# Performance work log

Hardware: AMD Instinct MI355X
Metric: run time of the kernel (lower is better)

Reference implementation:

```python
import jax, jax.numpy as jnp
import numpy as np

K = 16      # neighbors per node (hard-coded in ParticleNet)
EPS = 1e-5  # BatchNorm eps


def _forward(x, convs, fcW1, fcb1, fcW2, fcb2):
    # x: [B, N, F0]; convs: list of 3 layer-lists of (W, b, gamma, beta)
    B, N, _ = x.shape
    for c, layers in enumerate(convs):
        feat = x[..., :2] if c == 0 else x            # first kNN uses coords only
        sq = jnp.sum(feat * feat, axis=-1)            # [B, N]
        d2 = sq[:, :, None] + sq[:, None, :] - 2.0 * jnp.einsum('bnf,bmf->bnm', feat, feat)
        d2 = d2 + jnp.eye(N, dtype=d2.dtype) * 1e9    # exclude self-loops (knn_graph loop=False)
        idx = jax.lax.top_k(-d2, K)[1]                # [B, N, K] nearest-neighbor indices
        x_j = jax.vmap(lambda xb, ib: xb[ib])(x, idx) # gather neighbors -> [B, N, K, F]
        x_i = jnp.broadcast_to(x[:, :, None, :], x_j.shape)
        h = jnp.concatenate([x_i, x_j - x_i], axis=-1)  # PyG EdgeConv message input
        for (W, b, g, e) in layers:                   # Linear -> BatchNorm1d(train) -> ReLU
            h = h @ W + b
            m = h.mean(axis=(0, 1, 2))
            v = h.var(axis=(0, 1, 2))
            h = jax.nn.relu(g * (h - m) * jax.lax.rsqrt(v + EPS) + e)
        x = jnp.concatenate([h.mean(axis=2), x], axis=-1)  # aggr='mean', then skip-concat
    pooled = x.mean(axis=1)                           # global_mean_pool -> [B, 451]
    return (pooled @ fcW1 + fcb1) @ fcW2 + fcb2       # fc1 (no act) then fc2


def setup_inputs() -> dict:
    key = jax.random.key(0)
    B, N, F = 128, 128, 3
    ins, outs = [6, 134, 390], [64, 128, 256]
    d = {}
    ki = [0]
    def nk():
        ki[0] += 1
        return jax.random.fold_in(key, ki[0])
    d['x'] = jax.random.normal(nk(), (B, N, F), jnp.float32)
    for c in range(3):
        dims = [(ins[c], outs[c]), (outs[c], outs[c]), (outs[c], outs[c])]
        for l, (fi, fo) in enumerate(dims):
            d[f'W{c}{l}'] = jax.random.normal(nk(), (fi, fo), jnp.float32) / np.sqrt(fi).astype(np.float32)
            d[f'b{c}{l}'] = jnp.zeros((fo,), jnp.float32)
            d[f'g{c}{l}'] = jnp.ones((fo,), jnp.float32)
            d[f'e{c}{l}'] = jnp.zeros((fo,), jnp.float32)
    d['fcW1'] = jax.random.normal(nk(), (451, 256), jnp.float32) / np.float32(np.sqrt(451))
    d['fcb1'] = jnp.zeros((256,), jnp.float32)
    d['fcW2'] = jax.random.normal(nk(), (256, 5), jnp.float32) / np.float32(np.sqrt(256))
    d['fcb2'] = jnp.zeros((5,), jnp.float32)
    return d


def reference(x,
              W00, b00, g00, e00, W01, b01, g01, e01, W02, b02, g02, e02,
              W10, b10, g10, e10, W11, b11, g11, e11, W12, b12, g12, e12,
              W20, b20, g20, e20, W21, b21, g21, e21, W22, b22, g22, e22,
              fcW1, fcb1, fcW2, fcb2):
    convs = [
        [(W00, b00, g00, e00), (W01, b01, g01, e01), (W02, b02, g02, e02)],
        [(W10, b10, g10, e10), (W11, b11, g11, e11), (W12, b12, g12, e12)],
        [(W20, b20, g20, e20), (W21, b21, g21, e21), (W22, b22, g22, e22)],
    ]
    return _forward(x, convs, fcW1, fcb1, fcW2, fcb2)
```

## Files before the change

### kernel.cpp

```cpp
#include <hip/hip_runtime.h>
#include <hip/hip_bf16.h>
#include <type_traits>

typedef __hip_bfloat16 bf16;
typedef short v8s __attribute__((ext_vector_type(8)));
typedef short v2s __attribute__((ext_vector_type(2)));
typedef float v4f __attribute__((ext_vector_type(4)));

__device__ __forceinline__ float b2f(bf16 v) { return __bfloat162float(v); }
__device__ __forceinline__ bf16  f2b(float v) { return __float2bfloat16(v); }
__device__ __forceinline__ short f2bs(float v) {
    bf16 b = f2b(v); short s; __builtin_memcpy(&s, &b, 2); return s;
}
__device__ __forceinline__ float bs2f(short s) {
    bf16 b; __builtin_memcpy(&b, &s, 2); return b2f(b);
}

#define NB 128
#define NN 128
#define KNN 16
#define M_NODES (NB * NN)
#define NPOS ((long)M_NODES * KNN)
#define NREP 16

__device__ __forceinline__ void fold_stats(const float* __restrict__ st, int c,
                                           float& sum, float& sq) {
    sum = 0.f; sq = 0.f;
#pragma unroll
    for (int r = 0; r < NREP; ++r) { sum += st[r * 512 + c]; sq += st[r * 512 + 256 + c]; }
}

template<int TPB>
__device__ __forceinline__ int swz_tile(int bid) {
    int xcd = bid & 7;
    int slot = bid >> 3;
    int batch = xcd * 16 + slot / TPB;
    int tile = slot - (slot / TPB) * TPB;
    return batch * TPB + tile;
}

__global__ __launch_bounds__(256) void prep_kernel(
    const float* __restrict__ W0, const float* __restrict__ W1, const float* __restrict__ W2,
    short* __restrict__ W0d, short* __restrict__ W0b,
    short* __restrict__ W1b, short* __restrict__ W2b,
    float* __restrict__ stats, int F, int Fpad, int O)
{
    int i = blockIdx.x * 256 + threadIdx.x;
    const int nz = 3 * NREP * 512;
    if (i < nz) { stats[i] = 0.f; return; }
    i -= nz;
    const int n0 = O * Fpad;
    if (i < n0) {
        int c = i / Fpad, k = i - c * Fpad;
        if (k < F) {
            float wt = W0[(size_t)k * O + c];
            float wb = W0[(size_t)(F + k) * O + c];
            W0d[i] = f2bs(wt - wb);
            W0b[i] = f2bs(wb);
        } else { W0d[i] = 0; W0b[i] = 0; }
        return;
    }
    i -= n0;
    const int n1 = O * O;
    if (i < n1) {
        int c = i / O, k = i - c * O;
        W1b[i] = f2bs(W1[(size_t)k * O + c]);
        return;
    }
    i -= n1;
    if (i < n1) {
        int c = i / O, k = i - c * O;
        W2b[i] = f2bs(W2[(size_t)k * O + c]);
    }
}

__global__ __launch_bounds__(256) void dist_kernel(const float* __restrict__ x, int C, int D,
                                                   float* __restrict__ d2) {
    __shared__ float As[16][65];
    __shared__ float Bs[16][65];
    const int tid = threadIdx.x;
    const int tx = tid & 15, ty = tid >> 4;
    const int m0 = blockIdx.y * 64;
    const int b  = m0 >> 7;
    const int c0 = blockIdx.x * 64;
    float acc[4][4], rn[4], cn[4];
#pragma unroll
    for (int r = 0; r < 4; ++r) { rn[r] = 0.f; cn[r] = 0.f;
#pragma unroll
        for (int c = 0; c < 4; ++c) acc[r][c] = 0.f; }
    for (int k0 = 0; k0 < D; k0 += 16) {
        for (int l = tid; l < 1024; l += 256) {
            int k = l & 15, m = l >> 4;
            int kk = k0 + k;
            As[k][m] = (kk < D) ? x[(size_t)(m0 + m) * C + kk] : 0.f;
            Bs[k][m] = (kk < D) ? x[(size_t)(b * NN + c0 + m) * C + kk] : 0.f;
        }
        __syncthreads();
        for (int k = 0; k < 16; ++k) {
            float av[4], bv[4];
#pragma unroll
            for (int r = 0; r < 4; ++r) { av[r] = As[k][ty + 16 * r]; rn[r] += av[r] * av[r]; }
#pragma unroll
            for (int c = 0; c < 4; ++c) { bv[c] = Bs[k][tx + 16 * c]; cn[c] += bv[c] * bv[c]; }
#pragma unroll
            for (int r = 0; r < 4; ++r)
#pragma unroll
                for (int c = 0; c < 4; ++c) acc[r][c] += av[r] * bv[c];
        }
        __syncthreads();
    }
#pragma unroll
    for (int r = 0; r < 4; ++r)
#pragma unroll
        for (int c = 0; c < 4; ++c) {
            int m = m0 + ty + 16 * r;
            int jl = c0 + tx + 16 * c;
            int jg = b * NN + jl;
            float v = rn[r] + cn[c] - 2.0f * acc[r][c];
            if (m == jg) v += 1e9f;
            d2[(size_t)m * NN + jl] = v;
        }
}

__global__ __launch_bounds__(256) void knn_select_kernel(const float* __restrict__ d2,
                                                         int* __restrict__ idx) {
    const int node = blockIdx.x * 4 + (threadIdx.x >> 6);
    const int lane = threadIdx.x & 63;
    const float* row = d2 + (size_t)node * NN;
    float v0 = row[lane], v1 = row[lane + 64];
    int j0 = lane, j1 = lane + 64;
    int myIdx = 0;
#pragma unroll
    for (int k = 0; k < KNN; ++k) {
        float bv; int bj;
        if (v1 < v0 || (v1 == v0 && j1 < j0)) { bv = v1; bj = j1; }
        else                                 { bv = v0; bj = j0; }
#pragma unroll
        for (int off = 32; off; off >>= 1) {
            float ov = __shfl_xor(bv, off);
            int oj = __shfl_xor(bj, off);
            if (ov < bv || (ov == bv && oj < bj)) { bv = ov; bj = oj; }
        }
        if (bj == j0) v0 = 3.0e38f;
        if (bj == j1) v1 = 3.0e38f;
        if (lane == k) myIdx = bj;
    }
    if (lane < KNN) idx[(size_t)node * KNN + lane] = myIdx;
}

template<int O>
__global__ __launch_bounds__(256, 2) void node_gemm_mfma(
    const float* __restrict__ x, int F, int Fpad,
    const short* __restrict__ Wd, const short* __restrict__ Wb,
    const float* __restrict__ bias,
    float* __restrict__ T1, float* __restrict__ T2)
{
    constexpr int CPW = O / 64;
    __shared__ __align__(16) short Am[64][232];
    const int tid = threadIdx.x;
    const int lane = tid & 63, wave = tid >> 6;
    const int l15 = lane & 15, quad = lane >> 4;
    const int m0 = blockIdx.x * 64;
    for (int l = tid; l < 64 * Fpad; l += 256) {
        int m = l / Fpad, k = l - m * Fpad;
        Am[m][k] = (k < F) ? f2bs(x[(size_t)(m0 + m) * F + k]) : (short)0;
    }
    __syncthreads();
#pragma unroll
    for (int p = 0; p < 2; ++p) {
        const short* __restrict__ Wg = p ? Wb : Wd;
        float* __restrict__ T = p ? T2 : T1;
        v4f acc[4][CPW];
#pragma unroll
        for (int rt = 0; rt < 4; ++rt)
#pragma unroll
            for (int j = 0; j < CPW; ++j)
#pragma unroll
                for (int r = 0; r < 4; ++r) acc[rt][j][r] = 0.f;
        for (int k0 = 0; k0 < Fpad; k0 += 32) {
#pragma unroll
            for (int rt = 0; rt < 4; ++rt) {
                v8s av = *(const v8s*)&Am[rt * 16 + l15][k0 + quad * 8];
#pragma unroll
                for (int j = 0; j < CPW; ++j) {
                    int c = (wave * CPW + j) * 16 + l15;
                    v8s bv = *(const v8s*)&Wg[(size_t)c * Fpad + k0 + quad * 8];
                    acc[rt][j] = __builtin_amdgcn_mfma_f32_16x16x32_bf16(av, bv, acc[rt][j], 0, 0, 0);
                }
            }
        }
#pragma unroll
        for (int j = 0; j < CPW; ++j) {
            int c = (wave * CPW + j) * 16 + l15;
            float bb = p ? 0.f : bias[c];
#pragma unroll
            for (int rt = 0; rt < 4; ++rt)
#pragma unroll
                for (int r = 0; r < 4; ++r)
                    T[(size_t)(m0 + rt * 16 + quad * 4 + r) * O + c] = acc[rt][j][r] + bb;
        }
    }
}

template<int O>
__global__ __launch_bounds__(256) void stats0_lds_kernel(
    const float* __restrict__ T1, const float* __restrict__ T2,
    const int* __restrict__ idx, float* __restrict__ st0)
{
    constexpr int CH = (O > 128) ? 128 : O;
    constexpr int NG = 256 / CH;
    constexpr int NPG = NN / NG;
    __shared__ float T2s[NN][CH];
    __shared__ int idxs[NN * KNN];
    __shared__ float redS[NG][CH], redQ[NG][CH];
    const int tid = threadIdx.x;
    const int nchunk = O / CH;
    const int b = blockIdx.x / nchunk;
    const int c0 = (blockIdx.x - b * nchunk) * CH;
    const int rep = blockIdx.x & (NREP - 1);

    for (int l = tid; l < NN * CH; l += 256) {
        int n = l / CH, c = l - n * CH;
        T2s[n][c] = T2[(size_t)(b * NN + n) * O + c0 + c];
    }
    for (int l = tid; l < NN * KNN; l += 256) idxs[l] = idx[(size_t)b * NN * KNN + l];
    __syncthreads();

    const int c = tid & (CH - 1);
    const int g = tid / CH;
    float s = 0.f, q = 0.f;
    for (int n = g * NPG; n < (g + 1) * NPG; ++n) {
        float t1 = T1[(size_t)(b * NN + n) * O + c0 + c];
#pragma unroll
        for (int k = 0; k < KNN; ++k) {
            int j = idxs[n * KNN + k];
            float v = t1 + T2s[j][c];
            s += v; q += v * v;
        }
    }
    redS[g][c] = s; redQ[g][c] = q;
    __syncthreads();
    if (g == 0) {
#pragma unroll
        for (int gg = 1; gg < NG; ++gg) { s += redS[gg][c]; q += redQ[gg][c]; }
        atomicAdd(&st0[rep * 512 + c0 + c], s);
        atomicAdd(&st0[rep * 512 + 256 + c0 + c], q);
    }
}


template<int O, int ROWS>
__global__ __launch_bounds__(256, 4) void gemm1_kernel(
    const float* __restrict__ T1, const float* __restrict__ T2, const int* __restrict__ idx,
    const short* __restrict__ W1, const float* __restrict__ bias1,
    const float* __restrict__ gm0, const float* __restrict__ bt0,
    const float* __restrict__ st0, float* __restrict__ st1,
    short* __restrict__ h, float inv_n)
{
    constexpr int CPW = O / 64;
    constexpr int RT = ROWS / 16;
    constexpr int OSH = (O == 64) ? 6 : (O == 128 ? 7 : 8);
    constexpr int AP = O + 8;
    constexpr int TPB = 2048 / ROWS;
    __shared__ __align__(16) short Am[ROWS][AP];
    __shared__ float sc0[O], sh0[O];
    __shared__ int gArr[ROWS];
    const int tid = threadIdx.x;
    const int lane = tid & 63, wave = tid >> 6;
    const int l15 = lane & 15, quad = lane >> 4;
    const int work = swz_tile<TPB>(blockIdx.x);
    const int e0 = work * ROWS;
    const int nb0 = e0 >> 4;
    const int rep = work & (NREP - 1);

    for (int l = tid; l < ROWS; l += 256) {
        int e = e0 + l;
        int nd = e >> 4;
        gArr[l] = ((nd >> 7) << 7) + idx[e];
    }
    if (tid < O) {
        float sum, sq;
        fold_stats(st0, tid, sum, sq);
        float mean = sum * inv_n;
        float var = fmaxf(sq * inv_n - mean * mean, 0.f);
        float s = rsqrtf(var + 1e-5f) * gm0[tid];
        sc0[tid] = s; sh0[tid] = bt0[tid] - mean * s;
    }
    __syncthreads();

    for (int l = tid; l < ROWS * O / 2; l += 256) {
        int m = l >> (OSH - 1);
        int c = (l & (O / 2 - 1)) * 2;
        const float2 t1 = *(const float2*)&T1[(size_t)(nb0 + (m >> 4)) * O + c];
        const float2 t2 = *(const float2*)&T2[(size_t)gArr[m] * O + c];
        float v0 = fmaxf((t1.x + t2.x) * sc0[c] + sh0[c], 0.f);
        float v1 = fmaxf((t1.y + t2.y) * sc0[c + 1] + sh0[c + 1], 0.f);
        v2s pr; pr[0] = f2bs(v0); pr[1] = f2bs(v1);
        *(v2s*)&Am[m][c] = pr;
    }
    __syncthreads();

    v4f acc[RT][CPW];
#pragma unroll
    for (int rt = 0; rt < RT; ++rt)
#pragma unroll
        for (int j = 0; j < CPW; ++j)
#pragma unroll
            for (int r = 0; r < 4; ++r) acc[rt][j][r] = 0.f;

    v8s bvc[CPW];
#pragma unroll
    for (int j = 0; j < CPW; ++j) {
        int c = (wave * CPW + j) * 16 + l15;
        bvc[j] = *(const v8s*)&W1[(size_t)c * O + quad * 8];
    }
#pragma unroll
    for (int k0 = 0; k0 < O; k0 += 32) {
        v8s bvn[CPW];
        if (k0 + 32 < O) {
#pragma unroll
            for (int j = 0; j < CPW; ++j) {
                int c = (wave * CPW + j) * 16 + l15;
                bvn[j] = *(const v8s*)&W1[(size_t)c * O + k0 + 32 + quad * 8];
            }
        }
#pragma unroll
        for (int rt = 0; rt < RT; ++rt) {
            v8s av = *(const v8s*)&Am[rt * 16 + l15][k0 + quad * 8];
#pragma unroll
            for (int j = 0; j < CPW; ++j)
                acc[rt][j] = __builtin_amdgcn_mfma_f32_16x16x32_bf16(av, bvc[j], acc[rt][j], 0, 0, 0);
        }
        if (k0 + 32 < O) {
#pragma unroll
            for (int j = 0; j < CPW; ++j) bvc[j] = bvn[j];
        }
    }
#pragma unroll
    for (int j = 0; j < CPW; ++j) {
        float bb = bias1[(wave * CPW + j) * 16 + l15];
#pragma unroll
        for (int rt = 0; rt < RT; ++rt)
#pragma unroll
            for (int r = 0; r < 4; ++r) acc[rt][j][r] += bb;
    }
#pragma unroll
    for (int j = 0; j < CPW; ++j) {
        int c = (wave * CPW + j) * 16 + l15;
        float s = 0.f, q = 0.f;
#pragma unroll
        for (int rt = 0; rt < RT; ++rt)
#pragma unroll
            for (int r = 0; r < 4; ++r) { float v = acc[rt][j][r]; s += v; q += v * v; }
        s += __shfl_down(s, 32); s += __shfl_down(s, 16);
        q += __shfl_down(q, 32); q += __shfl_down(q, 16);
        if (quad == 0) { atomicAdd(&st1[rep * 512 + c], s); atomicAdd(&st1[rep * 512 + 256 + c], q); }
    }
    __syncthreads();
#pragma unroll
    for (int j = 0; j < CPW; ++j) {
        int c = (wave * CPW + j) * 16 + l15;
#pragma unroll
        for (int rt = 0; rt < RT; ++rt)
#pragma unroll
            for (int r = 0; r < 4; ++r)
                Am[rt * 16 + quad * 4 + r][c] = f2bs(acc[rt][j][r]);
    }
    __syncthreads();
    for (int g = tid; g < ROWS * O / 8; g += 256) {
        int row = g >> (OSH - 3);
        int c8 = (g & (O / 8 - 1)) * 8;
        *(v8s*)&h[(size_t)(e0 + row) * O + c8] = *(const v8s*)&Am[row][c8];
    }
}

template<int O, int ROWS>
__global__ __launch_bounds__(256, 4) void gemm2_kernel(
    short* __restrict__ h,
    const short* __restrict__ W2, const float* __restrict__ bias2,
    const float* __restrict__ gm1, const float* __restrict__ bt1,
    const float* __restrict__ st1, float* __restrict__ st2, float inv_n)
{
    constexpr int CPW = O / 64;
    constexpr int RT = ROWS / 16;
    constexpr int OSH = (O == 64) ? 6 : (O == 128 ? 7 : 8);
    constexpr int AP = O + 8;
    constexpr int TPB = 2048 / ROWS;
    __shared__ __align__(16) short Am[ROWS][AP];
    __shared__ float sc1[O], sh1[O];
    const int tid = threadIdx.x;
    const int lane = tid & 63, wave = tid >> 6;
    const int l15 = lane & 15, quad = lane >> 4;
    const int work = swz_tile<TPB>(blockIdx.x);
    const int e0 = work * ROWS;
    const int rep = work & (NREP - 1);

    if (tid < O) {
        float sum, sq;
        fold_stats(st1, tid, sum, sq);
        float mean = sum * inv_n;
        float var = fmaxf(sq * inv_n - mean * mean, 0.f);
        float s = rsqrtf(var + 1e-5f) * gm1[tid];
        sc1[tid] = s; sh1[tid] = bt1[tid] - mean * s;
    }
    __syncthreads();

    for (int g = tid; g < ROWS * O / 8; g += 256) {
        int row = g >> (OSH - 3);
        int c8 = (g & (O / 8 - 1)) * 8;
        v8s hv = *(const v8s*)&h[(size_t)(e0 + row) * O + c8];
        v8s ov;
#pragma unroll
        for (int j = 0; j < 8; ++j) {
            float v = bs2f(hv[j]) * sc1[c8 + j] + sh1[c8 + j];
            ov[j] = f2bs(fmaxf(v, 0.f));
        }
        *(v8s*)&Am[row][c8] = ov;
    }
    __syncthreads();

    v4f acc[RT][CPW];
#pragma unroll
    for (int rt = 0; rt < RT; ++rt)
#pragma unroll
        for (int j = 0; j < CPW; ++j)
#pragma unroll
            for (int r = 0; r < 4; ++r) acc[rt][j][r] = 0.f;

    v8s bvc[CPW];
#pragma unroll
    for (int j = 0; j < CPW; ++j) {
        int c = (wave * CPW + j) * 16 + l15;
        bvc[j] = *(const v8s*)&W2[(size_t)c * O + quad * 8];
    }
#pragma unroll
    for (int k0 = 0; k0 < O; k0 += 32) {
        v8s bvn[CPW];
        if (k0 + 32 < O) {
#pragma unroll
            for (int j = 0; j < CPW; ++j) {
                int c = (wave * CPW + j) * 16 + l15;
                bvn[j] = *(const v8s*)&W2[(size_t)c * O + k0 + 32 + quad * 8];
            }
        }
#pragma unroll
        for (int rt = 0; rt < RT; ++rt) {
            v8s av = *(const v8s*)&Am[rt * 16 + l15][k0 + quad * 8];
#pragma unroll
            for (int j = 0; j < CPW; ++j)
                acc[rt][j] = __builtin_amdgcn_mfma_f32_16x16x32_bf16(av, bvc[j], acc[rt][j], 0, 0, 0);
        }
        if (k0 + 32 < O) {
#pragma unroll
            for (int j = 0; j < CPW; ++j) bvc[j] = bvn[j];
        }
    }
#pragma unroll
    for (int j = 0; j < CPW; ++j) {
        float bb = bias2[(wave * CPW + j) * 16 + l15];
#pragma unroll
        for (int rt = 0; rt < RT; ++rt)
#pragma unroll
            for (int r = 0; r < 4; ++r) acc[rt][j][r] += bb;
    }
#pragma unroll
    for (int j = 0; j < CPW; ++j) {
        int c = (wave * CPW + j) * 16 + l15;
        float s = 0.f, q = 0.f;
#pragma unroll
        for (int rt = 0; rt < RT; ++rt)
#pragma unroll
            for (int r = 0; r < 4; ++r) { float v = acc[rt][j][r]; s += v; q += v * v; }
        s += __shfl_down(s, 32); s += __shfl_down(s, 16);
        q += __shfl_down(q, 32); q += __shfl_down(q, 16);
        if (quad == 0) { atomicAdd(&st2[rep * 512 + c], s); atomicAdd(&st2[rep * 512 + 256 + c], q); }
    }
    __syncthreads();
#pragma unroll
    for (int j = 0; j < CPW; ++j) {
        int c = (wave * CPW + j) * 16 + l15;
#pragma unroll
        for (int rt = 0; rt < RT; ++rt)
#pragma unroll
            for (int r = 0; r < 4; ++r)
                Am[rt * 16 + quad * 4 + r][c] = f2bs(acc[rt][j][r]);
    }
    __syncthreads();
    for (int g = tid; g < ROWS * O / 8; g += 256) {
        int row = g >> (OSH - 3);
        int c8 = (g & (O / 8 - 1)) * 8;
        *(v8s*)&h[(size_t)(e0 + row) * O + c8] = *(const v8s*)&Am[row][c8];
    }
}

template<int O, int ROWS>
__global__ __launch_bounds__(256) void finish_kernel(
    const short* __restrict__ h,
    const float* __restrict__ st2, const float* __restrict__ gm2, const float* __restrict__ bt2,
    const float* __restrict__ xold, float* __restrict__ xnew, int F, float inv_n)
{
    constexpr int G = 256 / O;
    constexpr int RPG = ROWS / G;
    constexpr int NPG = RPG / 16;
    constexpr int NPB = ROWS / 16;
    constexpr int TPB = 2048 / ROWS;
    const int tid = threadIdx.x;
    const int c = tid & (O - 1);
    const int rg = tid / O;
    const int work = swz_tile<TPB>(blockIdx.x);
    const int e0 = work * ROWS;
    const int nb0 = e0 >> 4;
    float sum, sq;
    fold_stats(st2, c, sum, sq);
    float mean = sum * inv_n;
    float var = fmaxf(sq * inv_n - mean * mean, 0.f);
    float sc = rsqrtf(var + 1e-5f) * gm2[c];
    float sh = bt2[c] - mean * sc;
    float s[NPG];
#pragma unroll
    for (int i = 0; i < NPG; ++i) s[i] = 0.f;
    const int m0 = rg * RPG;
#pragma unroll
    for (int r = 0; r < RPG; ++r) {
        float v = bs2f(h[(size_t)(e0 + m0 + r) * O + c]) * sc + sh;
        s[r >> 4] += fmaxf(v, 0.f);
    }
    const int Cnew = O + F;
#pragma unroll
    for (int i = 0; i < NPG; ++i)
        xnew[(size_t)(nb0 + rg * NPG + i) * Cnew + c] = s[i] * (1.0f / 16.0f);
    for (int l = tid; l < NPB * F; l += 256) {
        int nd = l / F, cc = l - nd * F;
        xnew[(size_t)(nb0 + nd) * Cnew + O + cc] = xold[(size_t)(nb0 + nd) * F + cc];
    }
}

__global__ __launch_bounds__(256) void pool_kernel(const float* __restrict__ x, float* __restrict__ pooled, int C) {
    int b = blockIdx.x, t = threadIdx.x;
    for (int c = t; c < C; c += 256) {
        float s = 0.f;
        for (int n = 0; n < NN; ++n) s += x[(size_t)(b * NN + n) * C + c];
        pooled[b * C + c] = s * (1.0f / NN);
    }
}

__global__ __launch_bounds__(256) void fc_kernel(const float* __restrict__ pooled,
                                                 const float* __restrict__ W1, const float* __restrict__ b1,
                                                 const float* __restrict__ W2, const float* __restrict__ b2,
                                                 float* __restrict__ out, int C) {
    __shared__ float px[451];
    __shared__ float h1[256];
    int b = blockIdx.x, t = threadIdx.x;
    for (int c = t; c < C; c += 256) px[c] = pooled[b * C + c];
    __syncthreads();
    float s = 0.f;
    for (int i = 0; i < C; ++i) s += px[i] * W1[(size_t)i * 256 + t];
    h1[t] = s + b1[t];
    __syncthreads();
    if (t < 5) {
        float s2 = 0.f;
        for (int j = 0; j < 256; ++j) s2 += h1[j] * W2[j * 5 + t];
        out[b * 5 + t] = s2 + b2[t];
    }
}

extern "C" void kernel_launch(void* const* d_in, const int* in_sizes, int n_in,
                              void* d_out, int out_size, void* d_ws, size_t ws_size,
                              hipStream_t stream) {
    const float* xin = (const float*)d_in[0];
    auto Wp = [&](int c, int l) { return (const float*)d_in[1 + c * 12 + l * 4 + 0]; };
    auto Bp = [&](int c, int l) { return (const float*)d_in[1 + c * 12 + l * 4 + 1]; };
    auto Gp = [&](int c, int l) { return (const float*)d_in[1 + c * 12 + l * 4 + 2]; };
    auto Ep = [&](int c, int l) { return (const float*)d_in[1 + c * 12 + l * 4 + 3]; };
    const float* fcW1 = (const float*)d_in[37];
    const float* fcb1 = (const float*)d_in[38];
    const float* fcW2 = (const float*)d_in[39];
    const float* fcb2 = (const float*)d_in[40];

    char* ws = (char*)d_ws;
    size_t off = 0;
    auto alloc = [&](size_t bytes) -> void* {
        void* p = ws + off;
        off += (bytes + 255) & ~(size_t)255;
        return p;
    };
    const int M = M_NODES;
    float* x1     = (float*)alloc((size_t)M * 67 * 4);
    float* x2     = (float*)alloc((size_t)M * 195 * 4);
    float* x3     = (float*)alloc((size_t)M * 451 * 4);
    float* T1     = (float*)alloc((size_t)M * 256 * 4);
    float* T2     = (float*)alloc((size_t)M * 256 * 4);
    int*   idxb   = (int*)alloc((size_t)M * KNN * 4);
    float* stats  = (float*)alloc((size_t)3 * NREP * 512 * 4);
    float* pooled = (float*)alloc((size_t)NB * 451 * 4);
    short* W1b    = (short*)alloc(256 * 256 * 2);
    short* W2b    = (short*)alloc(256 * 256 * 2);
    short* W0d    = (short*)alloc(256 * 224 * 2);
    short* W0b    = (short*)alloc(256 * 224 * 2);
    float* d2buf  = (float*)alloc((size_t)M * NN * 4);
    short* hbuf   = (short*)alloc((size_t)NPOS * 256 * 2);
    (void)in_sizes; (void)n_in; (void)out_size; (void)ws_size;

    float* st0 = stats;
    float* st1 = stats + NREP * 512;
    float* st2 = stats + 2 * NREP * 512;
    const float inv_n = 1.0f / (float)NPOS;

    auto run_conv = [&](const float* xc, float* xn, int F, int D, int O, int c) {
        const int Fpad = (F + 31) & ~31;
        dist_kernel<<<dim3(2, M / 64), 256, 0, stream>>>(xc, F, D, d2buf);
        knn_select_kernel<<<M / 4, 256, 0, stream>>>(d2buf, idxb);
        const int prepN = 3 * NREP * 512 + O * Fpad + 2 * O * O;
        prep_kernel<<<(prepN + 255) / 256, 256, 0, stream>>>(Wp(c, 0), Wp(c, 1), Wp(c, 2),
            W0d, W0b, W1b, W2b, stats, F, Fpad, O);
        auto launch = [&](auto tag) {
            constexpr int OO = decltype(tag)::value;
            constexpr int RR = 16384 / OO;
            const int grid = (int)(NPOS / RR);
            node_gemm_mfma<OO><<<M / 64, 256, 0, stream>>>(xc, F, Fpad, W0d, W0b, Bp(c, 0), T1, T2);
            stats0_lds_kernel<OO><<<NB * (OO > 128 ? 2 : 1), 256, 0, stream>>>(T1, T2, idxb, st0);
            gemm1_kernel<OO, RR><<<grid, 256, 0, stream>>>(T1, T2, idxb, W1b, Bp(c, 1),
                Gp(c, 0), Ep(c, 0), st0, st1, hbuf, inv_n);
            gemm2_kernel<OO, RR><<<grid, 256, 0, stream>>>(hbuf, W2b, Bp(c, 2),
                Gp(c, 1), Ep(c, 1), st1, st2, inv_n);
            finish_kernel<OO, RR><<<grid, 256, 0, stream>>>(hbuf, st2, Gp(c, 2), Ep(c, 2),
                xc, xn, F, inv_n);
        };
        if (O == 64)       launch(std::integral_constant<int, 64>{});
        else if (O == 128) launch(std::integral_constant<int, 128>{});
        else               launch(std::integral_constant<int, 256>{});
    };

    run_conv(xin, x1, 3, 2, 64, 0);
    run_conv(x1, x2, 67, 67, 128, 1);
    run_conv(x2, x3, 195, 195, 256, 2);
    pool_kernel<<<NB, 256, 0, stream>>>(x3, pooled, 451);
    fc_kernel<<<NB, 256, 0, stream>>>(pooled, fcW1, fcb1, fcW2, fcb2, (float*)d_out, 451);
}
```

Baseline: 870.9 us.

## Fuse distance and kNN selection per graph; shrink GEMM row tiles and raise occupancy

Merges the pairwise distance kernel and the top-k selection into one kernel per graph, keeping the 128x128 distance matrix in LDS so it is never written to or re-read from global memory. It also halves the rows per block in the EdgeConv GEMM kernels, raises their launch-bounds occupancy hint from 4 to 6, and drops the register double-buffering of weight fragments. The fused kNN kernel runs only 128 blocks with 64KB+ of LDS each and computes four tiles serially, which may underuse the GPU. Smaller tiles mean more blocks and more reloads of the weight fragments.

```diff
diff --git a/kernel.cpp b/kernel.cpp
--- a/kernel.cpp
+++ b/kernel.cpp
@@ -74,78 +74,81 @@
     }
 }
 
-__global__ __launch_bounds__(256) void dist_kernel(const float* __restrict__ x, int C, int D,
-                                                   float* __restrict__ d2) {
+__global__ __launch_bounds__(256) void knn_fused_kernel(const float* __restrict__ x,
+        int C, int D, int* __restrict__ idx) {
+    __shared__ float d2s[128][128];
     __shared__ float As[16][65];
     __shared__ float Bs[16][65];
     const int tid = threadIdx.x;
     const int tx = tid & 15, ty = tid >> 4;
-    const int m0 = blockIdx.y * 64;
-    const int b  = m0 >> 7;
-    const int c0 = blockIdx.x * 64;
-    float acc[4][4], rn[4], cn[4];
-#pragma unroll
-    for (int r = 0; r < 4; ++r) { rn[r] = 0.f; cn[r] = 0.f;
-#pragma unroll
-        for (int c = 0; c < 4; ++c) acc[r][c] = 0.f; }
-    for (int k0 = 0; k0 < D; k0 += 16) {
-        for (int l = tid; l < 1024; l += 256) {
-            int k = l & 15, m = l >> 4;
-            int kk = k0 + k;
-            As[k][m] = (kk < D) ? x[(size_t)(m0 + m) * C + kk] : 0.f;
-            Bs[k][m] = (kk < D) ? x[(size_t)(b * NN + c0 + m) * C + kk] : 0.f;
-        }
-        __syncthreads();
-        for (int k = 0; k < 16; ++k) {
-            float av[4], bv[4];
-#pragma unroll
-            for (int r = 0; r < 4; ++r) { av[r] = As[k][ty + 16 * r]; rn[r] += av[r] * av[r]; }
-#pragma unroll
-            for (int c = 0; c < 4; ++c) { bv[c] = Bs[k][tx + 16 * c]; cn[c] += bv[c] * bv[c]; }
+    const int b = blockIdx.x;
+#pragma unroll
+    for (int tr = 0; tr < 2; ++tr)
+#pragma unroll
+        for (int tc = 0; tc < 2; ++tc) {
+            const int m0 = b * NN + tr * 64;
+            const int c0 = tc * 64;
+            float acc[4][4], rn[4], cn[4];
+#pragma unroll
+            for (int r = 0; r < 4; ++r) { rn[r] = 0.f; cn[r] = 0.f;
+#pragma unroll
+                for (int c = 0; c < 4; ++c) acc[r][c] = 0.f; }
+            for (int k0 = 0; k0 < D; k0 += 16) {
+                __syncthreads();
+                for (int l = tid; l < 1024; l += 256) {
+                    int k = l & 15, m = l >> 4;
+                    int kk = k0 + k;
+                    As[k][m] = (kk < D) ? x[(size_t)(m0 + m) * C + kk] : 0.f;
+                    Bs[k][m] = (kk < D) ? x[(size_t)(b * NN + c0 + m) * C + kk] : 0.f;
+                }
+                __syncthreads();
+                for (int k = 0; k < 16; ++k) {
+                    float av[4], bv[4];
+#pragma unroll
+                    for (int r = 0; r < 4; ++r) { av[r] = As[k][ty + 16 * r]; rn[r] += av[r] * av[r]; }
+#pragma unroll
+                    for (int c = 0; c < 4; ++c) { bv[c] = Bs[k][tx + 16 * c]; cn[c] += bv[c] * bv[c]; }
+#pragma unroll
+                    for (int r = 0; r < 4; ++r)
+#pragma unroll
+                        for (int c = 0; c < 4; ++c) acc[r][c] += av[r] * bv[c];
+                }
+            }
 #pragma unroll
             for (int r = 0; r < 4; ++r)
 #pragma unroll
-                for (int c = 0; c < 4; ++c) acc[r][c] += av[r] * bv[c];
-        }
-        __syncthreads();
-    }
-#pragma unroll
-    for (int r = 0; r < 4; ++r)
-#pragma unroll
-        for (int c = 0; c < 4; ++c) {
-            int m = m0 + ty + 16 * r;
-            int jl = c0 + tx + 16 * c;
-            int jg = b * NN + jl;
-            float v = rn[r] + cn[c] - 2.0f * acc[r][c];
-            if (m == jg) v += 1e9f;
-            d2[(size_t)m * NN + jl] = v;
-        }
-}
-
-__global__ __launch_bounds__(256) void knn_select_kernel(const float* __restrict__ d2,
-                                                         int* __restrict__ idx) {
-    const int node = blockIdx.x * 4 + (threadIdx.x >> 6);
-    const int lane = threadIdx.x & 63;
-    const float* row = d2 + (size_t)node * NN;
-    float v0 = row[lane], v1 = row[lane + 64];
-    int j0 = lane, j1 = lane + 64;
-    int myIdx = 0;
-#pragma unroll
-    for (int k = 0; k < KNN; ++k) {
-        float bv; int bj;
-        if (v1 < v0 || (v1 == v0 && j1 < j0)) { bv = v1; bj = j1; }
-        else                                 { bv = v0; bj = j0; }
-#pragma unroll
-        for (int off = 32; off; off >>= 1) {
-            float ov = __shfl_xor(bv, off);
-            int oj = __shfl_xor(bj, off);
-            if (ov < bv || (ov == bv && oj < bj)) { bv = ov; bj = oj; }
-        }
-        if (bj == j0) v0 = 3.0e38f;
-        if (bj == j1) v1 = 3.0e38f;
-        if (lane == k) myIdx = bj;
-    }
-    if (lane < KNN) idx[(size_t)node * KNN + lane] = myIdx;
+                for (int c = 0; c < 4; ++c) {
+                    int row = tr * 64 + ty + 16 * r;
+                    int col = c0 + tx + 16 * c;
+                    float v = rn[r] + cn[c] - 2.0f * acc[r][c];
+                    if (row == col) v += 1e9f;
+                    d2s[row][col] = v;
+                }
+        }
+    __syncthreads();
+    const int lane = tid & 63, wave = tid >> 6;
+    for (int i = 0; i < 32; ++i) {
+        const int node = wave * 32 + i;
+        float v0 = d2s[node][lane], v1 = d2s[node][lane + 64];
+        int j0 = lane, j1 = lane + 64;
+        int myIdx = 0;
+#pragma unroll
+        for (int k = 0; k < KNN; ++k) {
+            float bv; int bj;
+            if (v1 < v0 || (v1 == v0 && j1 < j0)) { bv = v1; bj = j1; }
+            else                                 { bv = v0; bj = j0; }
+#pragma unroll
+            for (int off = 32; off; off >>= 1) {
+                float ov = __shfl_xor(bv, off);
+                int oj = __shfl_xor(bj, off);
+                if (ov < bv || (ov == bv && oj < bj)) { bv = ov; bj = oj; }
+            }
+            if (bj == j0) v0 = 3.0e38f;
+            if (bj == j1) v1 = 3.0e38f;
+            if (lane == k) myIdx = bj;
+        }
+        if (lane < KNN) idx[(size_t)(b * NN + node) * KNN + lane] = myIdx;
+    }
 }
 
 template<int O>
@@ -250,7 +253,7 @@
 
 
 template<int O, int ROWS>
-__global__ __launch_bounds__(256, 4) void gemm1_kernel(
+__global__ __launch_bounds__(256, 6) void gemm1_kernel(
     const float* __restrict__ T1, const float* __restrict__ T2, const int* __restrict__ idx,
     const short* __restrict__ W1, const float* __restrict__ bias1,
     const float* __restrict__ gm0, const float* __restrict__ bt0,
@@ -308,32 +311,20 @@
 #pragma unroll
             for (int r = 0; r < 4; ++r) acc[rt][j][r] = 0.f;
 
-    v8s bvc[CPW];
-#pragma unroll
-    for (int j = 0; j < CPW; ++j) {
-        int c = (wave * CPW + j) * 16 + l15;
-        bvc[j] = *(const v8s*)&W1[(size_t)c * O + quad * 8];
-    }
 #pragma unroll
     for (int k0 = 0; k0 < O; k0 += 32) {
-        v8s bvn[CPW];
-        if (k0 + 32 < O) {
-#pragma unroll
-            for (int j = 0; j < CPW; ++j) {
-                int c = (wave * CPW + j) * 16 + l15;
-                bvn[j] = *(const v8s*)&W1[(size_t)c * O + k0 + 32 + quad * 8];
-            }
+        v8s bv[CPW];
+#pragma unroll
+        for (int j = 0; j < CPW; ++j) {
+            int c = (wave * CPW + j) * 16 + l15;
+            bv[j] = *(const v8s*)&W1[(size_t)c * O + k0 + quad * 8];
         }
 #pragma unroll
         for (int rt = 0; rt < RT; ++rt) {
             v8s av = *(const v8s*)&Am[rt * 16 + l15][k0 + quad * 8];
 #pragma unroll
             for (int j = 0; j < CPW; ++j)
-                acc[rt][j] = __builtin_amdgcn_mfma_f32_16x16x32_bf16(av, bvc[j], acc[rt][j], 0, 0, 0);
-        }
-        if (k0 + 32 < O) {
-#pragma unroll
-            for (int j = 0; j < CPW; ++j) bvc[j] = bvn[j];
+                acc[rt][j] = __builtin_amdgcn_mfma_f32_16x16x32_bf16(av, bv[j], acc[rt][j], 0, 0, 0);
         }
     }
 #pragma unroll
@@ -375,7 +366,7 @@
 }
 
 template<int O, int ROWS>
-__global__ __launch_bounds__(256, 4) void gemm2_kernel(
+__global__ __launch_bounds__(256, 6) void gemm2_kernel(
     short* __restrict__ h,
     const short* __restrict__ W2, const float* __restrict__ bias2,
     const float* __restrict__ gm1, const float* __restrict__ bt1,
@@ -427,32 +418,20 @@
 #pragma unroll
             for (int r = 0; r < 4; ++r) acc[rt][j][r] = 0.f;
 
-    v8s bvc[CPW];
-#pragma unroll
-    for (int j = 0; j < CPW; ++j) {
-        int c = (wave * CPW + j) * 16 + l15;
-        bvc[j] = *(const v8s*)&W2[(size_t)c * O + quad * 8];
-    }
 #pragma unroll
     for (int k0 = 0; k0 < O; k0 += 32) {
-        v8s bvn[CPW];
-        if (k0 + 32 < O) {
-#pragma unroll
-            for (int j = 0; j < CPW; ++j) {
-                int c = (wave * CPW + j) * 16 + l15;
-                bvn[j] = *(const v8s*)&W2[(size_t)c * O + k0 + 32 + quad * 8];
-            }
+        v8s bv[CPW];
+#pragma unroll
+        for (int j = 0; j < CPW; ++j) {
+            int c = (wave * CPW + j) * 16 + l15;
+            bv[j] = *(const v8s*)&W2[(size_t)c * O + k0 + quad * 8];
         }
 #pragma unroll
         for (int rt = 0; rt < RT; ++rt) {
             v8s av = *(const v8s*)&Am[rt * 16 + l15][k0 + quad * 8];
 #pragma unroll
             for (int j = 0; j < CPW; ++j)
-                acc[rt][j] = __builtin_amdgcn_mfma_f32_16x16x32_bf16(av, bvc[j], acc[rt][j], 0, 0, 0);
-        }
-        if (k0 + 32 < O) {
-#pragma unroll
-            for (int j = 0; j < CPW; ++j) bvc[j] = bvn[j];
+                acc[rt][j] = __builtin_amdgcn_mfma_f32_16x16x32_bf16(av, bv[j], acc[rt][j], 0, 0, 0);
         }
     }
 #pragma unroll
@@ -597,7 +576,6 @@
     short* W2b    = (short*)alloc(256 * 256 * 2);
     short* W0d    = (short*)alloc(256 * 224 * 2);
     short* W0b    = (short*)alloc(256 * 224 * 2);
-    float* d2buf  = (float*)alloc((size_t)M * NN * 4);
     short* hbuf   = (short*)alloc((size_t)NPOS * 256 * 2);
     (void)in_sizes; (void)n_in; (void)out_size; (void)ws_size;
 
@@ -608,14 +586,13 @@
 
     auto run_conv = [&](const float* xc, float* xn, int F, int D, int O, int c) {
         const int Fpad = (F + 31) & ~31;
-        dist_kernel<<<dim3(2, M / 64), 256, 0, stream>>>(xc, F, D, d2buf);
-        knn_select_kernel<<<M / 4, 256, 0, stream>>>(d2buf, idxb);
+        knn_fused_kernel<<<NB, 256, 0, stream>>>(xc, F, D, idxb);
         const int prepN = 3 * NREP * 512 + O * Fpad + 2 * O * O;
         prep_kernel<<<(prepN + 255) / 256, 256, 0, stream>>>(Wp(c, 0), Wp(c, 1), Wp(c, 2),
             W0d, W0b, W1b, W2b, stats, F, Fpad, O);
         auto launch = [&](auto tag) {
             constexpr int OO = decltype(tag)::value;
-            constexpr int RR = 16384 / OO;
+            constexpr int RR = 8192 / OO;
             const int grid = (int)(NPOS / RR);
             node_gemm_mfma<OO><<<M / 64, 256, 0, stream>>>(xc, F, Fpad, W0d, W0b, Bp(c, 0), T1, T2);
             stats0_lds_kernel<OO><<<NB * (OO > 128 ? 2 : 1), 256, 0, stream>>>(T1, T2, idxb, st0);
```

Result: slower. 1.702 ms (+95.4%).
